# Kernel optimization log

Hardware: AMD Instinct MI355X
Metric: run time of the kernel (lower is better)

The kernel has to match this reference:

```python
import jax, jax.numpy as jnp
import numpy as np

EMBED_DIM = 768
N_HEADS = 12
TIME_RATIO = 0.5
HEAD_DIM = EMBED_DIM // N_HEADS          # 64
T_HEAD = int(HEAD_DIM * TIME_RATIO)      # 32 time dims per head
T_DIM = T_HEAD * N_HEADS                 # 384 time dims overall
EPS = 1e-5


def _ln(v, g, b):
    m = jnp.mean(v, axis=-1, keepdims=True)
    var = jnp.mean((v - m) ** 2, axis=-1, keepdims=True)
    return (v - m) * jax.lax.rsqrt(var + EPS) * g + b


def minkowski_ln(x, g_t, b_t, g_s, b_s):
    # normalize time-like and space-like channel groups separately
    xt, xs = x[..., :T_DIM], x[..., T_DIM:]
    return jnp.concatenate([_ln(xt, g_t, b_t), _ln(xs, g_s, b_s)], axis=-1)


def lorentz_attention(x, Wq, bq, Wk, bk, Wv, bv, Wo, bo):
    B, S, D = x.shape
    def heads(W, b):
        return (x @ W + b).reshape(B, S, N_HEADS, HEAD_DIM).transpose(0, 2, 1, 3)
    q, k, v = heads(Wq, bq), heads(Wk, bk), heads(Wv, bv)
    # Minkowski metric signature (-,...,-,+,...,+) within each head
    eta = jnp.concatenate([-jnp.ones((T_HEAD,), x.dtype), jnp.ones((HEAD_DIM - T_HEAD,), x.dtype)])
    logits = jnp.einsum('bhqd,bhkd->bhqk', q * eta, k) / np.sqrt(HEAD_DIM).astype(np.float32)
    attn = jax.nn.softmax(logits, axis=-1)
    o = jnp.einsum('bhqk,bhkd->bhqd', attn, v)
    o = o.transpose(0, 2, 1, 3).reshape(B, S, D)
    return o @ Wo + bo


def setup_inputs() -> dict:
    key = jax.random.key(0)
    ks = jax.random.split(key, 16)
    D, H4 = EMBED_DIM, EMBED_DIM * 4
    s = 0.02
    inp = {
        'x': jax.random.normal(ks[0], (2, 2048, D), jnp.float32),
        'Wq': jax.random.normal(ks[1], (D, D), jnp.float32) * s, 'bq': jnp.zeros((D,), jnp.float32),
        'Wk': jax.random.normal(ks[2], (D, D), jnp.float32) * s, 'bk': jnp.zeros((D,), jnp.float32),
        'Wv': jax.random.normal(ks[3], (D, D), jnp.float32) * s, 'bv': jnp.zeros((D,), jnp.float32),
        'Wo': jax.random.normal(ks[4], (D, D), jnp.float32) * s, 'bo': jnp.zeros((D,), jnp.float32),
        'g1t': jnp.ones((T_DIM,), jnp.float32), 'b1t': jnp.zeros((T_DIM,), jnp.float32),
        'g1s': jnp.ones((D - T_DIM,), jnp.float32), 'b1s': jnp.zeros((D - T_DIM,), jnp.float32),
        'W1': jax.random.normal(ks[5], (D, H4), jnp.float32) * s, 'bb1': jnp.zeros((H4,), jnp.float32),
        'W2': jax.random.normal(ks[6], (H4, D), jnp.float32) * s, 'bb2': jnp.zeros((D,), jnp.float32),
        'g2t': jnp.ones((T_DIM,), jnp.float32), 'b2t': jnp.zeros((T_DIM,), jnp.float32),
        'g2s': jnp.ones((D - T_DIM,), jnp.float32), 'b2s': jnp.zeros((D - T_DIM,), jnp.float32),
    }
    return inp


def reference(x, Wq, bq, Wk, bk, Wv, bv, Wo, bo,
              g1t, b1t, g1s, b1s, W1, bb1, W2, bb2,
              g2t, b2t, g2s, b2s):
    a = lorentz_attention(x, Wq, bq, Wk, bk, Wv, bv, Wo, bo)
    x = minkowski_ln(x + a, g1t, b1t, g1s, b1s)
    h = jax.nn.gelu(x @ W1 + bb1) @ W2 + bb2
    x = minkowski_ln(x + h, g2t, b2t, g2s, b2s)
    return x
```

## Files before the change

kernel.cpp:

```cpp
#include <hip/hip_runtime.h>
#include <cstddef>
#include <cstdint>

#define D_EMB  768
#define NHEAD  12
#define HDIM   64
#define THEAD  32
#define SEQ    2048
#define BATCH  2
#define NROW   (BATCH*SEQ)
#define HID4   3072

typedef unsigned short u16;
typedef __bf16 bf16x8 __attribute__((ext_vector_type(8)));
typedef float  f32x4  __attribute__((ext_vector_type(4)));
typedef float  f32x16 __attribute__((ext_vector_type(16)));
typedef unsigned short u16x8 __attribute__((ext_vector_type(8)));

__device__ __forceinline__ u16 f2bf(float f) {
    unsigned u = __builtin_bit_cast(unsigned, f);
    return (u16)((u + 0x7FFFu + ((u >> 16) & 1u)) >> 16);
}
__device__ __forceinline__ float bf2f(u16 h) {
    return __builtin_bit_cast(float, (unsigned)h << 16);
}
__device__ __forceinline__ u16 cvt_bf(float f) {
    return __builtin_bit_cast(u16, (__bf16)f);
}

__device__ __forceinline__ void gload_lds16(const void* g, void* l) {
    __builtin_amdgcn_global_load_lds(
        reinterpret_cast<const __attribute__((address_space(1))) void*>(
            reinterpret_cast<uintptr_t>(g)),
        reinterpret_cast<__attribute__((address_space(3))) void*>(
            (uint32_t)reinterpret_cast<uintptr_t>(l)),
        16, 0, 0);
}

__device__ __forceinline__ void tcast(float (*t)[33], const float* __restrict__ W,
                                      u16* __restrict__ WT, int K, int M,
                                      int mt, int kt)
{
    const int m0 = mt * 32, k0 = kt * 32;
    const int tx = threadIdx.x & 31, ty = threadIdx.x >> 5;
#pragma unroll
    for (int i = 0; i < 32; i += 8)
        t[ty + i][tx] = W[(size_t)(k0 + ty + i) * M + m0 + tx];
    __syncthreads();
#pragma unroll
    for (int i = 0; i < 32; i += 8)
        WT[(size_t)(m0 + ty + i) * K + k0 + tx] = f2bf(t[tx][ty + i]);
}

__global__ __launch_bounds__(256)
void prep(const float* __restrict__ Wq, const float* __restrict__ Wk,
          const float* __restrict__ Wv, const float* __restrict__ Wo,
          const float* __restrict__ W1, const float* __restrict__ W2,
          const float* __restrict__ bq, const float* __restrict__ bk,
          const float* __restrict__ bv, const float* __restrict__ x,
          u16* __restrict__ WqkvoT, u16* __restrict__ W1T,
          u16* __restrict__ W2T, u16* __restrict__ xb,
          float* __restrict__ bqkv)
{
    __shared__ float t[32][33];
    const int bid = blockIdx.x;
    if (bid < 2304) {
        const int z = bid / 576, r = bid % 576;
        const float* W = z == 0 ? Wq : z == 1 ? Wk : z == 2 ? Wv : Wo;
        tcast(t, W, WqkvoT + (size_t)z * 768 * 768, 768, 768, r % 24, r / 24);
    } else if (bid < 4608) {
        const int r = bid - 2304;
        tcast(t, W1, W1T, 768, 3072, r % 96, r / 96);
    } else if (bid < 6912) {
        const int r = bid - 4608;
        tcast(t, W2, W2T, 3072, 768, r % 24, r / 24);
    } else if (bid < 8448) {
        const int i = (bid - 6912) * 2048 + threadIdx.x * 8;
        const float4 a = *reinterpret_cast<const float4*>(x + i);
        const float4 b = *reinterpret_cast<const float4*>(x + i + 4);
        u16x8 h;
        h[0] = f2bf(a.x); h[1] = f2bf(a.y); h[2] = f2bf(a.z); h[3] = f2bf(a.w);
        h[4] = f2bf(b.x); h[5] = f2bf(b.y); h[6] = f2bf(b.z); h[7] = f2bf(b.w);
        *reinterpret_cast<u16x8*>(xb + i) = h;
    } else {
        const int i = (bid - 8448) * 256 + threadIdx.x;
        if (i < 2304)
            bqkv[i] = i < 768 ? bq[i] : (i < 1536 ? bk[i - 768] : bv[i - 1536]);
    }
}

template<int EPI>
__global__ __launch_bounds__(256)
void gemm_bf16(const u16* __restrict__ A, const u16* __restrict__ B,
               const float* __restrict__ bias, void* __restrict__ Cp,
               u16* __restrict__ VTp, int K, int N)
{
    __shared__ u16 As[2][128 * 32];
    __shared__ u16 Bs[2][128 * 32];
    const int tid  = threadIdx.x;
    const int lane = tid & 63;
    const int w    = tid >> 6;
    const int m0 = blockIdx.x * 128, n0 = blockIdx.y * 128;
    const int wr = (w >> 1) << 6, wc = (w & 1) << 6;

    const int seg0 = (w << 11) + lane * 16;
    const int row0 = seg0 >> 6, cb0 = (seg0 & 63) >> 1;
    const int seg1 = seg0 + 1024;
    const int row1 = seg1 >> 6, cb1 = (seg1 & 63) >> 1;
    const u16* a0 = A + (size_t)(m0 + row0) * K + cb0;
    const u16* a1 = A + (size_t)(m0 + row1) * K + cb1;
    const u16* b0 = B + (size_t)(n0 + row0) * K + cb0;
    const u16* b1 = B + (size_t)(n0 + row1) * K + cb1;
    const int lo0 = (w * 2 + 0) << 9;
    const int lo1 = (w * 2 + 1) << 9;

    int aIdx[4], bIdx[4];
#pragma unroll
    for (int i = 0; i < 4; ++i) {
        aIdx[i] = (wr + i * 16 + (lane & 15)) * 32 + ((lane >> 4) << 3);
        bIdx[i] = (wc + i * 16 + (lane & 15)) * 32 + ((lane >> 4) << 3);
    }

    f32x4 acc[4][4];
#pragma unroll
    for (int i = 0; i < 4; ++i)
#pragma unroll
        for (int j = 0; j < 4; ++j)
#pragma unroll
            for (int q = 0; q < 4; ++q) acc[i][j][q] = 0.f;

    gload_lds16(a0, &As[0][lo0]);
    gload_lds16(a1, &As[0][lo1]);
    gload_lds16(b0, &Bs[0][lo0]);
    gload_lds16(b1, &Bs[0][lo1]);
    __syncthreads();

    int cur = 0;
    for (int k0 = 0; k0 < K; k0 += 32) {
        if (k0 + 32 < K) {
            gload_lds16(a0 + k0 + 32, &As[cur ^ 1][lo0]);
            gload_lds16(a1 + k0 + 32, &As[cur ^ 1][lo1]);
            gload_lds16(b0 + k0 + 32, &Bs[cur ^ 1][lo0]);
            gload_lds16(b1 + k0 + 32, &Bs[cur ^ 1][lo1]);
        }
        bf16x8 af[4], bv[4];
#pragma unroll
        for (int i = 0; i < 4; ++i)
            af[i] = *reinterpret_cast<const bf16x8*>(&As[cur][aIdx[i]]);
#pragma unroll
        for (int j = 0; j < 4; ++j)
            bv[j] = *reinterpret_cast<const bf16x8*>(&Bs[cur][bIdx[j]]);
#pragma unroll
        for (int i = 0; i < 4; ++i)
#pragma unroll
            for (int j = 0; j < 4; ++j)
                acc[i][j] = __builtin_amdgcn_mfma_f32_16x16x32_bf16(
                    af[i], bv[j], acc[i][j], 0, 0, 0);
        __syncthreads();
        cur ^= 1;
    }

#pragma unroll
    for (int i = 0; i < 4; ++i) {
#pragma unroll
        for (int q = 0; q < 4; ++q) {
            const int row = m0 + wr + i * 16 + ((lane >> 4) << 2) + q;
#pragma unroll
            for (int j = 0; j < 4; ++j) {
                const int col = n0 + wc + j * 16 + (lane & 15);
                float v = acc[i][j][q] + bias[col];
                if (EPI == 2) {
                    const float z = 1.5957691216057308f *
                                    (v + 0.044715f * v * v * v);
                    const float e = __builtin_amdgcn_exp2f(z * -1.4426950408889634f);
                    v = v * __builtin_amdgcn_rcpf(1.f + e);
                    ((u16*)Cp)[(size_t)row * N + col] = cvt_bf(v);
                } else {
                    if (n0 < 1536) {
                        ((u16*)Cp)[(size_t)row * 1536 + col] = cvt_bf(v);
                    } else {
                        const int c2 = col - 1536;
                        const int hh = c2 >> 6, dd = c2 & 63;
                        const int bb = row >> 11, tok = row & 2047;
                        VTp[((size_t)(bb * NHEAD + hh) * HDIM + dd) * SEQ + tok]
                            = cvt_bf(v);
                    }
                }
            }
        }
    }
}

__global__ __launch_bounds__(256)
void gemm_n64(const u16* __restrict__ A, const u16* __restrict__ B,
              const float* __restrict__ bias, float* __restrict__ C0,
              float* __restrict__ C1, int Khalf, int Ktot, int N)
{
    __shared__ u16 As[2][64 * 32];
    __shared__ u16 Bs[2][128 * 32];
    const int tid  = threadIdx.x;
    const int lane = tid & 63;
    const int w    = tid >> 6;
    const int l15  = lane & 15;
    const int g    = lane >> 4;
    const int m0 = blockIdx.x * 64, n0 = blockIdx.y * 128;
    const int zz = blockIdx.z;
    const int kbase = zz * Khalf;
    float* __restrict__ C = zz ? C1 : C0;

    const int segA = (w << 10) + lane * 16;
    const int rowA = segA >> 6, cbA = (segA & 63) >> 1;
    const u16* aP = A + (size_t)(m0 + rowA) * Ktot + kbase + cbA;
    const int loA = w << 9;
    const int seg0 = (w << 11) + lane * 16;
    const int row0 = seg0 >> 6, cb0 = (seg0 & 63) >> 1;
    const int seg1 = seg0 + 1024;
    const int row1 = seg1 >> 6, cb1 = (seg1 & 63) >> 1;
    const u16* b0 = B + (size_t)(n0 + row0) * Ktot + kbase + cb0;
    const u16* b1 = B + (size_t)(n0 + row1) * Ktot + kbase + cb1;
    const int lo0 = w << 10, lo1 = (w << 10) + 512;

    int aIdx[4], bIdx[2];
#pragma unroll
    for (int i = 0; i < 4; ++i) aIdx[i] = (i * 16 + l15) * 32 + (g << 3);
#pragma unroll
    for (int j = 0; j < 2; ++j) bIdx[j] = ((w << 5) + j * 16 + l15) * 32 + (g << 3);

    f32x4 acc[4][2];
#pragma unroll
    for (int i = 0; i < 4; ++i)
#pragma unroll
        for (int j = 0; j < 2; ++j)
#pragma unroll
            for (int q = 0; q < 4; ++q) acc[i][j][q] = 0.f;

    gload_lds16(aP, &As[0][loA]);
    gload_lds16(b0, &Bs[0][lo0]);
    gload_lds16(b1, &Bs[0][lo1]);
    __syncthreads();

    int cur = 0;
    for (int k0 = 0; k0 < Khalf; k0 += 32) {
        if (k0 + 32 < Khalf) {
            gload_lds16(aP + k0 + 32, &As[cur ^ 1][loA]);
            gload_lds16(b0 + k0 + 32, &Bs[cur ^ 1][lo0]);
            gload_lds16(b1 + k0 + 32, &Bs[cur ^ 1][lo1]);
        }
        bf16x8 af[4], bv[2];
#pragma unroll
        for (int i = 0; i < 4; ++i)
            af[i] = *reinterpret_cast<const bf16x8*>(&As[cur][aIdx[i]]);
#pragma unroll
        for (int j = 0; j < 2; ++j)
            bv[j] = *reinterpret_cast<const bf16x8*>(&Bs[cur][bIdx[j]]);
#pragma unroll
        for (int i = 0; i < 4; ++i)
#pragma unroll
            for (int j = 0; j < 2; ++j)
                acc[i][j] = __builtin_amdgcn_mfma_f32_16x16x32_bf16(
                    af[i], bv[j], acc[i][j], 0, 0, 0);
        __syncthreads();
        cur ^= 1;
    }

#pragma unroll
    for (int i = 0; i < 4; ++i) {
#pragma unroll
        for (int q = 0; q < 4; ++q) {
            const int row = m0 + i * 16 + (g << 2) + q;
#pragma unroll
            for (int j = 0; j < 2; ++j) {
                const int col = n0 + (w << 5) + j * 16 + l15;
                const float bb = zz ? 0.f : bias[col];
                C[(size_t)row * N + col] = acc[i][j][q] + bb;
            }
        }
    }
}

#define SM_SCALE 0.18033688011112042f

__global__ __launch_bounds__(256)
void attn_mfma(const u16* __restrict__ QK, const u16* __restrict__ VT,
               u16* __restrict__ O0, u16* __restrict__ O1,
               float* __restrict__ Sp)
{
    __shared__ u16 Ks[2][64 * 64];
    __shared__ u16 Vs[2][64 * 64];
    __shared__ u16 Ps[128 * 72];

    const int tid  = threadIdx.x;
    const int lane = tid & 63;
    const int w    = tid >> 6;
    const int l31  = lane & 31;
    const int hi   = lane >> 5;
    const int bh   = blockIdx.x;
    const int b    = bh / NHEAD, h = bh % NHEAD;
    const int q0   = blockIdx.y * 128;
    const int z    = blockIdx.z;
    const int keybase = z * 1024;
    const int bS   = b * SEQ;

    bf16x8 bq[4];
    {
        const u16* Qg = QK + (size_t)(bS + q0 + w * 32 + l31) * 1536 + h * HDIM;
#pragma unroll
        for (int s = 0; s < 4; ++s) {
            const u16x8 hq = *reinterpret_cast<const u16x8*>(
                Qg + (s * 2 + hi) * 8);
            const float sc = (s < 2) ? -SM_SCALE : SM_SCALE;
            u16x8 hs;
#pragma unroll
            for (int j = 0; j < 8; ++j)
                hs[j] = cvt_bf(bf2f(hq[j]) * sc);
            bq[s] = __builtin_bit_cast(bf16x8, hs);
        }
    }

    const int rl = lane >> 3;
    const int cs = ((lane & 7) ^ rl) << 3;
    const u16* pK = QK + (size_t)(bS + keybase + 16 * w + rl) * 1536
                    + 768 + h * HDIM + cs;
    const u16* pV = VT + ((size_t)(b * NHEAD + h) * HDIM + 16 * w + rl) * SEQ
                    + keybase + cs;

    f32x16 accO[2];
#pragma unroll
    for (int dt = 0; dt < 2; ++dt)
#pragma unroll
        for (int r = 0; r < 16; ++r) accO[dt][r] = 0.f;
    float psum = 0.f;

#define ATTN_STAGE(c, kt)                                                   \
    do {                                                                    \
        u16* dK = &Ks[c][w * 1024];                                         \
        u16* dV = &Vs[c][w * 1024];                                         \
        gload_lds16(pK + (size_t)(kt) * 1536,       dK);                    \
        gload_lds16(pK + (size_t)((kt) + 8) * 1536, dK + 512);              \
        gload_lds16(pV + (kt),           dV);                               \
        gload_lds16(pV + (kt) + 8 * SEQ, dV + 512);                         \
    } while (0)

    ATTN_STAGE(0, 0);
    __syncthreads();
    int cur = 0;

    for (int kt = 0; kt < 1024; kt += 64) {
        if (kt + 64 < 1024) ATTN_STAGE(cur ^ 1, kt + 64);

        f32x16 sac[2];
        __builtin_amdgcn_s_setprio(1);
#pragma unroll
        for (int t = 0; t < 2; ++t) {
#pragma unroll
            for (int r = 0; r < 16; ++r) sac[t][r] = 0.f;
#pragma unroll
            for (int s = 0; s < 4; ++s) {
                const int key = t * 32 + l31;
                const int ch  = (s * 2 + hi) ^ (key & 7);
                const bf16x8 ak = *reinterpret_cast<const bf16x8*>(
                    &Ks[cur][key * 64 + ch * 8]);
                sac[t] = __builtin_amdgcn_mfma_f32_32x32x16_bf16(
                    ak, bq[s], sac[t], 0, 0, 0);
            }
        }
        __builtin_amdgcn_s_setprio(0);

        const int prow = (w * 32 + l31) * 72;
#pragma unroll
        for (int t = 0; t < 2; ++t) {
#pragma unroll
            for (int grp = 0; grp < 4; ++grp) {
                const float e0 = __builtin_amdgcn_exp2f(sac[t][grp * 4 + 0]);
                const float e1 = __builtin_amdgcn_exp2f(sac[t][grp * 4 + 1]);
                const float e2 = __builtin_amdgcn_exp2f(sac[t][grp * 4 + 2]);
                const float e3 = __builtin_amdgcn_exp2f(sac[t][grp * 4 + 3]);
                psum += (e0 + e1) + (e2 + e3);
                ushort4 pk4;
                pk4.x = cvt_bf(e0); pk4.y = cvt_bf(e1);
                pk4.z = cvt_bf(e2); pk4.w = cvt_bf(e3);
                const int key0 = t * 32 + grp * 8 + hi * 4;
                *reinterpret_cast<ushort4*>(&Ps[prow + key0]) = pk4;
            }
        }

        __builtin_amdgcn_s_setprio(1);
#pragma unroll
        for (int ks = 0; ks < 4; ++ks) {
            const bf16x8 ap = *reinterpret_cast<const bf16x8*>(
                &Ps[prow + (ks * 2 + hi) * 8]);
#pragma unroll
            for (int dt = 0; dt < 2; ++dt) {
                const int d  = dt * 32 + l31;
                const int ch = (ks * 2 + hi) ^ (d & 7);
                const bf16x8 bv = *reinterpret_cast<const bf16x8*>(
                    &Vs[cur][d * 64 + ch * 8]);
                accO[dt] = __builtin_amdgcn_mfma_f32_32x32x16_bf16(
                    ap, bv, accO[dt], 0, 0, 0);
            }
        }
        __builtin_amdgcn_s_setprio(0);
        __syncthreads();
        cur ^= 1;
    }

    psum += __shfl_xor(psum, 32);
    u16* __restrict__ Oz = z ? O1 : O0;
#pragma unroll
    for (int dt = 0; dt < 2; ++dt)
#pragma unroll
        for (int r = 0; r < 16; ++r) {
            const int qr = q0 + w * 32 + (r & 3) + 8 * (r >> 2) + 4 * hi;
            Oz[(size_t)(bS + qr) * D_EMB + h * HDIM + dt * 32 + l31]
                = cvt_bf(accO[dt][r]);
        }
    if (lane < 32)
        Sp[(size_t)z * (BATCH * NHEAD * SEQ) + (b * NHEAD + h) * SEQ
           + q0 + w * 32 + l31] = psum;
#undef ATTN_STAGE
}

__global__ __launch_bounds__(256)
void attn_merge(const u16* __restrict__ O0, const u16* __restrict__ O1,
                const float* __restrict__ Sp, u16* __restrict__ Ab)
{
    const int gid = blockIdx.x * 256 + threadIdx.x;
    const size_t e = (size_t)gid * 8;
    const int row = gid / 96;
    const int cc  = gid % 96;
    const int h   = cc >> 3;
    const int b   = row >> 11, q = row & 2047;
    const int si  = (b * NHEAD + h) * SEQ + q;
    const float s = Sp[si] + Sp[(size_t)(BATCH * NHEAD * SEQ) + si];
    const float inv = __builtin_amdgcn_rcpf(s);
    const u16x8 a = *reinterpret_cast<const u16x8*>(O0 + e);
    const u16x8 c = *reinterpret_cast<const u16x8*>(O1 + e);
    u16x8 o;
#pragma unroll
    for (int j = 0; j < 8; ++j)
        o[j] = cvt_bf((bf2f(a[j]) + bf2f(c[j])) * inv);
    *reinterpret_cast<u16x8*>(Ab + e) = o;
}

template<int XBF, int WF32>
__global__ __launch_bounds__(256)
void mink_ln(const void* __restrict__ Xp, const float* __restrict__ R1,
             const float* __restrict__ R2,
             const float* __restrict__ gt, const float* __restrict__ bt,
             const float* __restrict__ gs, const float* __restrict__ bs,
             float* __restrict__ Out, u16* __restrict__ OutB, int nrows)
{
    const int wid  = (int)((blockIdx.x * 256 + threadIdx.x) >> 6);
    const int lane = threadIdx.x & 63;
    const int row  = wid >> 1, half = wid & 1;
    if (row >= nrows) return;

    const float* g  = half ? gs : gt;
    const float* bb = half ? bs : bt;
    const size_t base = (size_t)row * D_EMB + half * 384;

    float v[6];
    float sum = 0.f;
#pragma unroll
    for (int i = 0; i < 6; ++i) {
        const size_t e = base + i * 64 + lane;
        const float xv = XBF ? bf2f(((const u16*)Xp)[e]) : ((const float*)Xp)[e];
        const float t = xv + R1[e] + R2[e];
        v[i] = t; sum += t;
    }
#pragma unroll
    for (int off = 32; off; off >>= 1) sum += __shfl_xor(sum, off);
    const float mean = sum * (1.f / 384.f);

    float ss = 0.f;
#pragma unroll
    for (int i = 0; i < 6; ++i) { const float d = v[i] - mean; ss += d * d; }
#pragma unroll
    for (int off = 32; off; off >>= 1) ss += __shfl_xor(ss, off);
    const float rstd = rsqrtf(ss * (1.f / 384.f) + 1e-5f);

#pragma unroll
    for (int i = 0; i < 6; ++i) {
        const int e = i * 64 + lane;
        const float o = (v[i] - mean) * rstd * g[e] + bb[e];
        if (WF32) Out[base + e] = o;
        if (OutB) OutB[base + e] = cvt_bf(o);
    }
}

extern "C" void kernel_launch(void* const* d_in, const int* in_sizes, int n_in,
                              void* d_out, int out_size, void* d_ws, size_t ws_size,
                              hipStream_t stream)
{
    const float* x   = (const float*)d_in[0];
    const float* Wq  = (const float*)d_in[1];
    const float* bq  = (const float*)d_in[2];
    const float* Wk  = (const float*)d_in[3];
    const float* bk  = (const float*)d_in[4];
    const float* Wv  = (const float*)d_in[5];
    const float* bv  = (const float*)d_in[6];
    const float* Wo  = (const float*)d_in[7];
    const float* bo  = (const float*)d_in[8];
    const float* g1t = (const float*)d_in[9];
    const float* b1t = (const float*)d_in[10];
    const float* g1s = (const float*)d_in[11];
    const float* b1s = (const float*)d_in[12];
    const float* W1  = (const float*)d_in[13];
    const float* bb1 = (const float*)d_in[14];
    const float* W2  = (const float*)d_in[15];
    const float* bb2 = (const float*)d_in[16];
    const float* g2t = (const float*)d_in[17];
    const float* b2t = (const float*)d_in[18];
    const float* g2s = (const float*)d_in[19];
    const float* b2s = (const float*)d_in[20];
    float* out = (float*)d_out;

    const size_t ND = (size_t)NROW * D_EMB;
    u16* WqkvoT = (u16*)d_ws;
    u16* W1T = WqkvoT + 2359296;
    u16* W2T = W1T + 2359296;
    u16* xb  = W2T + 2359296;
    u16* QKb = xb + ND;
    u16* VTb = QKb + (size_t)NROW * 1536;
    u16* Ab  = VTb + ND;
    u16* Hb  = QKb;
    float* QKf  = (float*)QKb;
    float* AoF  = (float*)(Ab + ND);
    float* bqkv = AoF;
    u16* Op0 = (u16*)AoF;
    u16* Op1 = Op0 + ND;
    float* Sp = (float*)xb;

    const dim3 blk(256);

    prep<<<8457, blk, 0, stream>>>(Wq, Wk, Wv, Wo, W1, W2, bq, bk, bv, x,
                                   WqkvoT, W1T, W2T, xb, bqkv);

    gemm_bf16<3><<<dim3(32, 18), blk, 0, stream>>>(xb, WqkvoT, bqkv, QKb, VTb,
                                                   768, 2304);
    attn_mfma<<<dim3(BATCH * NHEAD, SEQ / 128, 2), blk, 0, stream>>>(
        QKb, VTb, Op0, Op1, Sp);
    attn_merge<<<(int)(ND / 8 / 256), blk, 0, stream>>>(Op0, Op1, Sp, Ab);

    gemm_n64<<<dim3(64, 6, 2), blk, 0, stream>>>(
        Ab, WqkvoT + (size_t)2304 * 768, bo, AoF, QKf, 384, 768, 768);
    mink_ln<0, 0><<<2048, blk, 0, stream>>>(x, AoF, QKf, g1t, b1t, g1s, b1s,
                                            nullptr, xb, NROW);
    gemm_bf16<2><<<dim3(32, 24), blk, 0, stream>>>(xb, W1T, bb1, Hb, nullptr,
                                                   768, 3072);
    gemm_n64<<<dim3(64, 6, 2), blk, 0, stream>>>(
        Hb, W2T, bb2, AoF, out, 1536, 3072, 768);
    mink_ln<1, 1><<<2048, blk, 0, stream>>>(xb, AoF, out, g2t, b2t, g2s, b2s,
                                            out, nullptr, NROW);
}
```

Before: 183.9 us.

## Keep attention probabilities in registers and stage K/V through registers

The attention kernel no longer writes the softmax probabilities to the Ps shared buffer and reads them back. The S accumulator layout is reused directly as the A operand of the PV MFMA, with K and V loaded in a permuted key order so the reduction dimension still lines up. K/V tiles are now loaded from global memory into registers early in each step and written to LDS with an XOR swizzle at 8-byte granularity after compute, replacing the direct global-to-LDS loads. This removes the LDS round trip and a shared buffer, but adds register pressure and splits each LDS read into two 8-byte reads.

```diff
diff --git a/kernel.cpp b/kernel.cpp
--- a/kernel.cpp
+++ b/kernel.cpp
@@ -287,13 +287,13 @@
 {
     __shared__ u16 Ks[2][64 * 64];
     __shared__ u16 Vs[2][64 * 64];
-    __shared__ u16 Ps[128 * 72];
 
     const int tid  = threadIdx.x;
     const int lane = tid & 63;
     const int w    = tid >> 6;
     const int l31  = lane & 31;
     const int hi   = lane >> 5;
+    const int m15  = l31 & 15;
     const int bh   = blockIdx.x;
     const int b    = bh / NHEAD, h = bh % NHEAD;
     const int q0   = blockIdx.y * 128;
@@ -307,7 +307,7 @@
 #pragma unroll
         for (int s = 0; s < 4; ++s) {
             const u16x8 hq = *reinterpret_cast<const u16x8*>(
-                Qg + (s * 2 + hi) * 8);
+                Qg + s * 16 + hi * 8);
             const float sc = (s < 2) ? -SM_SCALE : SM_SCALE;
             u16x8 hs;
 #pragma unroll
@@ -317,12 +317,36 @@
         }
     }
 
-    const int rl = lane >> 3;
-    const int cs = ((lane & 7) ^ rl) << 3;
-    const u16* pK = QK + (size_t)(bS + keybase + 16 * w + rl) * 1536
-                    + 768 + h * HDIM + cs;
-    const u16* pV = VT + ((size_t)(b * NHEAD + h) * HDIM + 16 * w + rl) * SEQ
-                    + keybase + cs;
+    const int rj = lane >> 3, cj = lane & 7;
+    const int R0 = 16 * w + rj, R1 = R0 + 8;
+    const u16* gK0 = QK + (size_t)(bS + keybase + R0) * 1536 + 768 + h * HDIM + cj * 8;
+    const u16* gK1 = QK + (size_t)(bS + keybase + R1) * 1536 + 768 + h * HDIM + cj * 8;
+    const u16* gV0 = VT + ((size_t)(b * NHEAD + h) * HDIM + R0) * SEQ + keybase + cj * 8;
+    const u16* gV1 = VT + ((size_t)(b * NHEAD + h) * HDIM + R1) * SEQ + keybase + cj * 8;
+    const int wo00 = R0 * 64 + 4 * ((2 * cj + 0) ^ (R0 & 15));
+    const int wo01 = R0 * 64 + 4 * ((2 * cj + 1) ^ (R0 & 15));
+    const int wo10 = R1 * 64 + 4 * ((2 * cj + 0) ^ (R1 & 15));
+    const int wo11 = R1 * 64 + 4 * ((2 * cj + 1) ^ (R1 & 15));
+
+    uint4 sK0, sK1, sV0, sV1;
+#define LOADSTAGE(kt)                                                        \
+    do {                                                                     \
+        sK0 = *reinterpret_cast<const uint4*>(gK0 + (size_t)(kt) * 1536);    \
+        sK1 = *reinterpret_cast<const uint4*>(gK1 + (size_t)(kt) * 1536);    \
+        sV0 = *reinterpret_cast<const uint4*>(gV0 + (kt));                   \
+        sV1 = *reinterpret_cast<const uint4*>(gV1 + (kt));                   \
+    } while (0)
+#define WRITESTAGE(c)                                                        \
+    do {                                                                     \
+        *reinterpret_cast<uint2*>(&Ks[c][wo00]) = make_uint2(sK0.x, sK0.y);  \
+        *reinterpret_cast<uint2*>(&Ks[c][wo01]) = make_uint2(sK0.z, sK0.w);  \
+        *reinterpret_cast<uint2*>(&Ks[c][wo10]) = make_uint2(sK1.x, sK1.y);  \
+        *reinterpret_cast<uint2*>(&Ks[c][wo11]) = make_uint2(sK1.z, sK1.w);  \
+        *reinterpret_cast<uint2*>(&Vs[c][wo00]) = make_uint2(sV0.x, sV0.y);  \
+        *reinterpret_cast<uint2*>(&Vs[c][wo01]) = make_uint2(sV0.z, sV0.w);  \
+        *reinterpret_cast<uint2*>(&Vs[c][wo10]) = make_uint2(sV1.x, sV1.y);  \
+        *reinterpret_cast<uint2*>(&Vs[c][wo11]) = make_uint2(sV1.z, sV1.w);  \
+    } while (0)
 
     f32x16 accO[2];
 #pragma unroll
@@ -331,22 +355,13 @@
         for (int r = 0; r < 16; ++r) accO[dt][r] = 0.f;
     float psum = 0.f;
 
-#define ATTN_STAGE(c, kt)                                                   \
-    do {                                                                    \
-        u16* dK = &Ks[c][w * 1024];                                         \
-        u16* dV = &Vs[c][w * 1024];                                         \
-        gload_lds16(pK + (size_t)(kt) * 1536,       dK);                    \
-        gload_lds16(pK + (size_t)((kt) + 8) * 1536, dK + 512);              \
-        gload_lds16(pV + (kt),           dV);                               \
-        gload_lds16(pV + (kt) + 8 * SEQ, dV + 512);                         \
-    } while (0)
-
-    ATTN_STAGE(0, 0);
+    LOADSTAGE(0);
+    WRITESTAGE(0);
     __syncthreads();
     int cur = 0;
 
     for (int kt = 0; kt < 1024; kt += 64) {
-        if (kt + 64 < 1024) ATTN_STAGE(cur ^ 1, kt + 64);
+        if (kt + 64 < 1024) LOADSTAGE(kt + 64);
 
         f32x16 sac[2];
         __builtin_amdgcn_s_setprio(1);
@@ -354,52 +369,56 @@
         for (int t = 0; t < 2; ++t) {
 #pragma unroll
             for (int r = 0; r < 16; ++r) sac[t][r] = 0.f;
+            const int krow = (t * 32 + l31) * 64;
 #pragma unroll
             for (int s = 0; s < 4; ++s) {
-                const int key = t * 32 + l31;
-                const int ch  = (s * 2 + hi) ^ (key & 7);
-                const bf16x8 ak = *reinterpret_cast<const bf16x8*>(
-                    &Ks[cur][key * 64 + ch * 8]);
+                const int g0 = (4 * s + 2 * hi) ^ m15;
+                const uint2 ra = *reinterpret_cast<const uint2*>(
+                    &Ks[cur][krow + 4 * g0]);
+                const uint2 rb = *reinterpret_cast<const uint2*>(
+                    &Ks[cur][krow + 4 * (g0 ^ 1)]);
+                const bf16x8 ak = __builtin_bit_cast(
+                    bf16x8, make_uint4(ra.x, ra.y, rb.x, rb.y));
                 sac[t] = __builtin_amdgcn_mfma_f32_32x32x16_bf16(
                     ak, bq[s], sac[t], 0, 0, 0);
             }
         }
         __builtin_amdgcn_s_setprio(0);
 
-        const int prow = (w * 32 + l31) * 72;
-#pragma unroll
-        for (int t = 0; t < 2; ++t) {
-#pragma unroll
-            for (int grp = 0; grp < 4; ++grp) {
-                const float e0 = __builtin_amdgcn_exp2f(sac[t][grp * 4 + 0]);
-                const float e1 = __builtin_amdgcn_exp2f(sac[t][grp * 4 + 1]);
-                const float e2 = __builtin_amdgcn_exp2f(sac[t][grp * 4 + 2]);
-                const float e3 = __builtin_amdgcn_exp2f(sac[t][grp * 4 + 3]);
-                psum += (e0 + e1) + (e2 + e3);
-                ushort4 pk4;
-                pk4.x = cvt_bf(e0); pk4.y = cvt_bf(e1);
-                pk4.z = cvt_bf(e2); pk4.w = cvt_bf(e3);
-                const int key0 = t * 32 + grp * 8 + hi * 4;
-                *reinterpret_cast<ushort4*>(&Ps[prow + key0]) = pk4;
+        u16x8 pk[4];
+#pragma unroll
+        for (int t = 0; t < 2; ++t)
+#pragma unroll
+            for (int r = 0; r < 16; ++r) {
+                const float ev = __builtin_amdgcn_exp2f(sac[t][r]);
+                psum += ev;
+                pk[2 * t + (r >> 3)][r & 7] = cvt_bf(ev);
             }
-        }
 
         __builtin_amdgcn_s_setprio(1);
 #pragma unroll
-        for (int ks = 0; ks < 4; ++ks) {
-            const bf16x8 ap = *reinterpret_cast<const bf16x8*>(
-                &Ps[prow + (ks * 2 + hi) * 8]);
-#pragma unroll
-            for (int dt = 0; dt < 2; ++dt) {
-                const int d  = dt * 32 + l31;
-                const int ch = (ks * 2 + hi) ^ (d & 7);
-                const bf16x8 bv = *reinterpret_cast<const bf16x8*>(
-                    &Vs[cur][d * 64 + ch * 8]);
-                accO[dt] = __builtin_amdgcn_mfma_f32_32x32x16_bf16(
-                    ap, bv, accO[dt], 0, 0, 0);
+        for (int t = 0; t < 2; ++t)
+#pragma unroll
+            for (int u = 0; u < 2; ++u) {
+                const bf16x8 ap = __builtin_bit_cast(bf16x8, pk[2 * t + u]);
+#pragma unroll
+                for (int dt = 0; dt < 2; ++dt) {
+                    const int vrow = (dt * 32 + l31) * 64;
+                    const int g0 = (8 * t + 4 * u + hi) ^ m15;
+                    const int g1 = (8 * t + 4 * u + 2 + hi) ^ m15;
+                    const uint2 ra = *reinterpret_cast<const uint2*>(
+                        &Vs[cur][vrow + 4 * g0]);
+                    const uint2 rb = *reinterpret_cast<const uint2*>(
+                        &Vs[cur][vrow + 4 * g1]);
+                    const bf16x8 bv = __builtin_bit_cast(
+                        bf16x8, make_uint4(ra.x, ra.y, rb.x, rb.y));
+                    accO[dt] = __builtin_amdgcn_mfma_f32_32x32x16_bf16(
+                        ap, bv, accO[dt], 0, 0, 0);
+                }
             }
-        }
         __builtin_amdgcn_s_setprio(0);
+
+        if (kt + 64 < 1024) WRITESTAGE(cur ^ 1);
         __syncthreads();
         cur ^= 1;
     }
@@ -417,7 +436,8 @@
     if (lane < 32)
         Sp[(size_t)z * (BATCH * NHEAD * SEQ) + (b * NHEAD + h) * SEQ
            + q0 + w * 32 + l31] = psum;
-#undef ATTN_STAGE
+#undef LOADSTAGE
+#undef WRITESTAGE
 }
 
 __global__ __launch_bounds__(256)
```

New measurement: 192.7 us. 4.8% more time.

## Keep softmax probabilities in registers instead of staging through LDS

Applied to the files above, without the earlier changes.

The attention kernel no longer writes the exponentiated scores to a shared-memory P tile and reads them back. The QK^T MFMA accumulator layout is reused directly as the A operand of the PV MFMA. V is instead read as two 8-byte fragments per operand, matched to the permuted key order. This removes the LDS round trip and the shared buffer for P, at the cost of more, smaller LDS reads for V and a reliance on the key permutation being consistent.

```diff
diff --git a/kernel.cpp b/kernel.cpp
--- a/kernel.cpp
+++ b/kernel.cpp
@@ -287,7 +287,6 @@
 {
     __shared__ u16 Ks[2][64 * 64];
     __shared__ u16 Vs[2][64 * 64];
-    __shared__ u16 Ps[128 * 72];
 
     const int tid  = threadIdx.x;
     const int lane = tid & 63;
@@ -307,7 +306,7 @@
 #pragma unroll
         for (int s = 0; s < 4; ++s) {
             const u16x8 hq = *reinterpret_cast<const u16x8*>(
-                Qg + (s * 2 + hi) * 8);
+                Qg + s * 16 + hi * 8);
             const float sc = (s < 2) ? -SM_SCALE : SM_SCALE;
             u16x8 hs;
 #pragma unroll
@@ -354,51 +353,51 @@
         for (int t = 0; t < 2; ++t) {
 #pragma unroll
             for (int r = 0; r < 16; ++r) sac[t][r] = 0.f;
+            const int krow = (t * 32 + l31) * 64;
+            const int m7 = l31 & 7;
 #pragma unroll
             for (int s = 0; s < 4; ++s) {
-                const int key = t * 32 + l31;
-                const int ch  = (s * 2 + hi) ^ (key & 7);
                 const bf16x8 ak = *reinterpret_cast<const bf16x8*>(
-                    &Ks[cur][key * 64 + ch * 8]);
+                    &Ks[cur][krow + (((s * 2 + hi) ^ m7) << 3)]);
                 sac[t] = __builtin_amdgcn_mfma_f32_32x32x16_bf16(
                     ak, bq[s], sac[t], 0, 0, 0);
             }
         }
         __builtin_amdgcn_s_setprio(0);
 
-        const int prow = (w * 32 + l31) * 72;
-#pragma unroll
-        for (int t = 0; t < 2; ++t) {
-#pragma unroll
-            for (int grp = 0; grp < 4; ++grp) {
-                const float e0 = __builtin_amdgcn_exp2f(sac[t][grp * 4 + 0]);
-                const float e1 = __builtin_amdgcn_exp2f(sac[t][grp * 4 + 1]);
-                const float e2 = __builtin_amdgcn_exp2f(sac[t][grp * 4 + 2]);
-                const float e3 = __builtin_amdgcn_exp2f(sac[t][grp * 4 + 3]);
-                psum += (e0 + e1) + (e2 + e3);
-                ushort4 pk4;
-                pk4.x = cvt_bf(e0); pk4.y = cvt_bf(e1);
-                pk4.z = cvt_bf(e2); pk4.w = cvt_bf(e3);
-                const int key0 = t * 32 + grp * 8 + hi * 4;
-                *reinterpret_cast<ushort4*>(&Ps[prow + key0]) = pk4;
+        u16x8 pk[4];
+#pragma unroll
+        for (int t = 0; t < 2; ++t)
+#pragma unroll
+            for (int r = 0; r < 16; ++r) {
+                const float ev = __builtin_amdgcn_exp2f(sac[t][r]);
+                psum += ev;
+                pk[2 * t + (r >> 3)][r & 7] = cvt_bf(ev);
             }
-        }
 
         __builtin_amdgcn_s_setprio(1);
 #pragma unroll
-        for (int ks = 0; ks < 4; ++ks) {
-            const bf16x8 ap = *reinterpret_cast<const bf16x8*>(
-                &Ps[prow + (ks * 2 + hi) * 8]);
-#pragma unroll
-            for (int dt = 0; dt < 2; ++dt) {
-                const int d  = dt * 32 + l31;
-                const int ch = (ks * 2 + hi) ^ (d & 7);
-                const bf16x8 bv = *reinterpret_cast<const bf16x8*>(
-                    &Vs[cur][d * 64 + ch * 8]);
-                accO[dt] = __builtin_amdgcn_mfma_f32_32x32x16_bf16(
-                    ap, bv, accO[dt], 0, 0, 0);
+        for (int t = 0; t < 2; ++t)
+#pragma unroll
+            for (int u = 0; u < 2; ++u) {
+                const bf16x8 ap = __builtin_bit_cast(bf16x8, pk[2 * t + u]);
+#pragma unroll
+                for (int dt = 0; dt < 2; ++dt) {
+                    const int d = dt * 32 + l31;
+                    const int vrow = d * 64;
+                    const int d7 = d & 7;
+                    const int g0 = 2 * ((4 * t + 2 * u)     ^ d7) + hi;
+                    const int g1 = 2 * ((4 * t + 2 * u + 1) ^ d7) + hi;
+                    const uint2 ra = *reinterpret_cast<const uint2*>(
+                        &Vs[cur][vrow + 4 * g0]);
+                    const uint2 rb = *reinterpret_cast<const uint2*>(
+                        &Vs[cur][vrow + 4 * g1]);
+                    const bf16x8 bv = __builtin_bit_cast(
+                        bf16x8, make_uint4(ra.x, ra.y, rb.x, rb.y));
+                    accO[dt] = __builtin_amdgcn_mfma_f32_32x32x16_bf16(
+                        ap, bv, accO[dt], 0, 0, 0);
+                }
             }
-        }
         __builtin_amdgcn_s_setprio(0);
         __syncthreads();
         cur ^= 1;
```

Measured after the change: 183.5 us. No clear change (-0.2%).
